# Optimization experiments

Hardware: AMD Instinct MI355X
Metric: run time of the kernel (lower is better)

Reference implementation:

```python
import jax, jax.numpy as jnp
import numpy as np

N_ATOMS = 20000
N_EDGES = 80000
ATOM_DIM = 29
BOND_DIM = 11
UNITS = 64
STEPS = 4
PAD = UNITS - ATOM_DIM  # 35


def setup_inputs() -> dict:
    key = jax.random.key(0)
    ks = jax.random.split(key, 8)
    atom_features = jax.random.normal(ks[0], (N_ATOMS, ATOM_DIM), dtype=jnp.float32)
    bond_features = jax.random.normal(ks[1], (N_EDGES, BOND_DIM), dtype=jnp.float32)
    pi = jax.random.randint(ks[2], (N_EDGES, 2), 0, N_ATOMS, dtype=jnp.int32)
    # tf.math.segment_sum in the original requires sorted segment ids
    order = jnp.argsort(pi[:, 0])
    pair_indices = pi[order]
    scale = 0.05
    edge_kernel = jax.random.normal(ks[3], (BOND_DIM, UNITS * UNITS), dtype=jnp.float32) * scale
    edge_bias = jnp.zeros((UNITS * UNITS,), dtype=jnp.float32)
    gru_kernel = jax.random.normal(ks[4], (UNITS, 3 * UNITS), dtype=jnp.float32) * scale
    gru_rec_kernel = jax.random.normal(ks[5], (UNITS, 3 * UNITS), dtype=jnp.float32) * scale
    gru_bias = jnp.zeros((2, 3 * UNITS), dtype=jnp.float32)
    return {
        "atom_features": atom_features,
        "bond_features": bond_features,
        "pair_indices": pair_indices,
        "edge_kernel": edge_kernel,
        "edge_bias": edge_bias,
        "gru_kernel": gru_kernel,
        "gru_rec_kernel": gru_rec_kernel,
        "gru_bias": gru_bias,
    }


def _edge_network(h, bond_features, pair_indices, edge_kernel, edge_bias):
    # per-edge learned transform: [E, bond_dim] -> [E, d, d]
    bf = bond_features @ edge_kernel + edge_bias
    bf = bf.reshape(-1, UNITS, UNITS)
    nbr = h[pair_indices[:, 1]]                      # gather neighbors [E, d]
    transformed = jnp.einsum('eij,ej->ei', bf, nbr)  # per-edge matvec
    # aggregate messages at target atoms (segment_sum)
    return jax.ops.segment_sum(transformed, pair_indices[:, 0], num_segments=N_ATOMS)


def _gru_cell(x, h, kernel, rec_kernel, bias):
    # keras GRUCell, reset_after=True
    xm = x @ kernel + bias[0]        # [N, 3u]
    hm = h @ rec_kernel + bias[1]    # [N, 3u]
    xz, xr, xh = jnp.split(xm, 3, axis=-1)
    rz, rr, rh = jnp.split(hm, 3, axis=-1)
    z = jax.nn.sigmoid(xz + rz)
    r = jax.nn.sigmoid(xr + rr)
    hh = jnp.tanh(xh + r * rh)
    return z * h + (1.0 - z) * hh


def reference(atom_features, bond_features, pair_indices, edge_kernel, edge_bias,
              gru_kernel, gru_rec_kernel, gru_bias):
    h = jnp.pad(atom_features, ((0, 0), (0, PAD)))
    for _ in range(STEPS):
        msg = _edge_network(h, bond_features, pair_indices, edge_kernel, edge_bias)
        h = _gru_cell(msg, h, gru_kernel, gru_rec_kernel, gru_bias)
    return h
```

## Files before the change

### kernel.cpp

```cpp
#include <hip/hip_runtime.h>

#define N_ATOMS 20000
#define N_EDGES 80000
#define ATOM_DIM 29
#define BOND_DIM 11
#define UNITS 64
#define STEPS 4
#define GCOLS 768
#define KTOT  832
#define BM    16
#define NTH   256
#define ASTRIDE 836
#define CT_MAIN 12
#define KT_MAIN 26
#define CT_RH 4
#define KT_RH 2
#define GSTRIDE 193
#define RSTRIDE 65

typedef _Float16 f16;
typedef __attribute__((ext_vector_type(8))) _Float16 f16x8;
typedef __attribute__((ext_vector_type(4))) float f32x4;

__global__ void init_h(const float* __restrict__ atom, float* __restrict__ h,
                       f16* __restrict__ h16) {
    int idx = blockIdx.x*256 + threadIdx.x;
    if (idx >= N_ATOMS*UNITS) return;
    int a = idx >> 6, i = idx & 63;
    float v = (i < ATOM_DIM) ? atom[a*ATOM_DIM + i] : 0.f;
    h[idx] = v;
    h16[idx] = (f16)v;
}

__global__ void build_rowptr(const int* __restrict__ pair, int* __restrict__ row_ptr) {
    int e = blockIdx.x*256 + threadIdx.x;
    if (e >= N_EDGES) return;
    int s = pair[2*e];
    if (e == 0) for (int a = 0; a <= s; a++) row_ptr[a] = 0;
    int snext = (e == N_EDGES-1) ? N_ATOMS : pair[2*(e+1)];
    for (int a = s+1; a <= snext; a++) row_ptr[a] = e+1;
}

__global__ void build_w3m(const float* __restrict__ ek, const float* __restrict__ eb,
                          const float* __restrict__ gk, const float* __restrict__ grk,
                          const float* __restrict__ gb, f16* __restrict__ W3m,
                          float* __restrict__ bias2) {
    int idx = blockIdx.x*256 + threadIdx.x;
    if (idx < 256) {
        int comp = idx >> 6, i = idx & 63;
        float b;
        if (comp == 0)      b = gb[i]       + gb[192 + i];
        else if (comp == 1) b = gb[64 + i]  + gb[256 + i];
        else if (comp == 2) b = gb[128 + i];
        else                b = gb[320 + i];
        bias2[idx] = b;
    }
    if (idx >= CT_MAIN*KT_MAIN*512) return;
    int t = idx >> 9, rem = idx & 511;
    int ct = t / KT_MAIN, kt = t % KT_MAIN;
    int lane = rem >> 3, e = rem & 7;
    int lq = lane >> 4, lr = lane & 15;
    int col = ct*16 + lr;
    int comp = col >> 6, i = col & 63;
    int k = kt*32 + lq*8 + e;
    float val = 0.f;
    if (k < GCOLS) {
        int b = k >> 6, q = k & 63;
        const float* E = (b < BOND_DIM) ? (ek + (size_t)b*4096 + q) : (eb + q);
        const float* T = gk + comp*64 + i;
        #pragma unroll 8
        for (int m = 0; m < 64; m++) val += E[m*64] * T[m*192];
    } else {
        int j = k - GCOLS;
        if (comp < 2) val = grk[j*192 + comp*64 + i];
    }
    W3m[idx] = (f16)val;
}

__global__ void build_w3r(const float* __restrict__ grk, f16* __restrict__ W3r) {
    int idx = blockIdx.x*256 + threadIdx.x;
    if (idx >= CT_RH*KT_RH*512) return;
    int t = idx >> 9, rem = idx & 511;
    int rt = t / KT_RH, kt = t % KT_RH;
    int lane = rem >> 3, e = rem & 7;
    int lq = lane >> 4, lr = lane & 15;
    int i = rt*16 + lr;
    int j = kt*32 + lq*8 + e;
    W3r[idx] = (f16)grk[j*192 + 128 + i];
}

__global__ __launch_bounds__(NTH, 5) void fused_step(
    const int* __restrict__ pair, const int* __restrict__ row_ptr,
    const float* __restrict__ bond, const f16* __restrict__ h16_in,
    f16* __restrict__ h16_out, const f16* __restrict__ W3m,
    const f16* __restrict__ W3r, const float* __restrict__ bias2,
    float* __restrict__ h) {
  __shared__ __align__(16) char smem[BM*ASTRIDE*2];
  f16 (*As)[ASTRIDE] = (f16 (*)[ASTRIDE])smem;
  float (*gates)[GSTRIDE] = (float (*)[GSTRIDE])smem;
  float (*rhb)[RSTRIDE] = (float (*)[RSTRIDE])(smem + BM*GSTRIDE*4);

  int a0 = blockIdx.x * BM;
  int tid = threadIdx.x;
  int lane = tid & 63, w = tid >> 6;
  int lq = lane >> 4, lr = lane & 15;

  const f16* bp[4];
  if (w < 3) {
    #pragma unroll
    for (int n=0;n<4;n++)
      bp[n] = W3m + ((size_t)(w*4 + n)*KT_MAIN)*512 + lane*8;
  } else {
    #pragma unroll
    for (int n=0;n<4;n++)
      bp[n] = W3r + ((size_t)n*KT_RH)*512 + lane*8;
  }
  f16x8 pb[4][2];
  #pragma unroll
  for (int n=0;n<4;n++) {
    pb[n][0] = *(const f16x8*)(bp[n]);
    pb[n][1] = *(const f16x8*)(bp[n] + 512);
  }

  for (int t = 0; t < 4; t++) {
    int r = w*4 + t;
    int a = a0 + r;
    int s = row_ptr[a], e_end = row_ptr[a+1];
    float g[BOND_DIM+1];
    #pragma unroll
    for (int b=0;b<=BOND_DIM;b++) g[b] = 0.f;
    int e = s;
    for (; e + 1 < e_end; e += 2) {
      int d0 = pair[2*e+1], d1 = pair[2*e+3];
      float h0 = (float)h16_in[(size_t)d0*UNITS + lane];
      float h1 = (float)h16_in[(size_t)d1*UNITS + lane];
      g[BOND_DIM] += h0 + h1;
      #pragma unroll
      for (int b=0;b<BOND_DIM;b++)
        g[b] += bond[(size_t)e*BOND_DIM + b]*h0 + bond[(size_t)(e+1)*BOND_DIM + b]*h1;
    }
    if (e < e_end) {
      int d0 = pair[2*e+1];
      float h0 = (float)h16_in[(size_t)d0*UNITS + lane];
      g[BOND_DIM] += h0;
      #pragma unroll
      for (int b=0;b<BOND_DIM;b++) g[b] += bond[(size_t)e*BOND_DIM + b]*h0;
    }
    #pragma unroll
    for (int b=0;b<=BOND_DIM;b++) As[r][b*64 + lane] = (f16)g[b];
    As[r][GCOLS + lane] = h16_in[(size_t)a*UNITS + lane];
  }

  int ei = tid & 63;
  float bz  = bias2[ei];
  float br  = bias2[64 + ei];
  float bxh = bias2[128 + ei];
  float brh = bias2[192 + ei];
  float hold[4];
  #pragma unroll
  for (int p=0;p<4;p++)
    hold[p] = h[(size_t)(a0 + (tid >> 6) + p*4)*UNITS + ei];

  __syncthreads();

  f32x4 acc[4];
  #pragma unroll
  for (int n=0;n<4;n++) acc[n] = (f32x4){0.f,0.f,0.f,0.f};

  if (w < 3) {
    #pragma unroll 2
    for (int kt = 0; kt < KT_MAIN; kt++) {
      f16x8 af = *(const f16x8*)&As[lr][kt*32 + lq*8];
      acc[0] = __builtin_amdgcn_mfma_f32_16x16x32_f16(af, pb[0][kt&1], acc[0], 0, 0, 0);
      acc[1] = __builtin_amdgcn_mfma_f32_16x16x32_f16(af, pb[1][kt&1], acc[1], 0, 0, 0);
      acc[2] = __builtin_amdgcn_mfma_f32_16x16x32_f16(af, pb[2][kt&1], acc[2], 0, 0, 0);
      acc[3] = __builtin_amdgcn_mfma_f32_16x16x32_f16(af, pb[3][kt&1], acc[3], 0, 0, 0);
      if (kt + 2 < KT_MAIN) {
        #pragma unroll
        for (int n=0;n<4;n++)
          pb[n][kt&1] = *(const f16x8*)(bp[n] + (size_t)(kt+2)*512);
      }
    }
  } else {
    #pragma unroll
    for (int kt = 0; kt < KT_RH; kt++) {
      f16x8 af = *(const f16x8*)&As[lr][GCOLS + kt*32 + lq*8];
      acc[0] = __builtin_amdgcn_mfma_f32_16x16x32_f16(af, pb[0][kt], acc[0], 0, 0, 0);
      acc[1] = __builtin_amdgcn_mfma_f32_16x16x32_f16(af, pb[1][kt], acc[1], 0, 0, 0);
      acc[2] = __builtin_amdgcn_mfma_f32_16x16x32_f16(af, pb[2][kt], acc[2], 0, 0, 0);
      acc[3] = __builtin_amdgcn_mfma_f32_16x16x32_f16(af, pb[3][kt], acc[3], 0, 0, 0);
    }
  }
  __syncthreads();

  if (w < 3) {
    #pragma unroll
    for (int n=0;n<4;n++) {
      int col = (w*4+n)*16 + lr;
      #pragma unroll
      for (int rr=0;rr<4;rr++)
        gates[lq*4 + rr][col] = acc[n][rr];
    }
  } else {
    #pragma unroll
    for (int n=0;n<4;n++) {
      int col = n*16 + lr;
      #pragma unroll
      for (int rr=0;rr<4;rr++)
        rhb[lq*4 + rr][col] = acc[n][rr];
    }
  }
  __syncthreads();

  #pragma unroll
  for (int p=0;p<4;p++) {
    int a_loc = (tid >> 6) + p*4;
    int a = a0 + a_loc;
    float zs = gates[a_loc][ei]        + bz;
    float rs = gates[a_loc][64 + ei]   + br;
    float xh = gates[a_loc][128 + ei]  + bxh;
    float rh = rhb[a_loc][ei]          + brh;
    float z  = 1.f/(1.f + __expf(-zs));
    float rg = 1.f/(1.f + __expf(-rs));
    float hh = tanhf(xh + rg*rh);
    float hn = z*hold[p] + (1.f - z)*hh;
    h[(size_t)a*UNITS + ei] = hn;
    h16_out[(size_t)a*UNITS + ei] = (f16)hn;
  }
}

extern "C" void kernel_launch(void* const* d_in, const int* in_sizes, int n_in,
                              void* d_out, int out_size, void* d_ws, size_t ws_size,
                              hipStream_t stream) {
  const float* atom  = (const float*)d_in[0];
  const float* bond  = (const float*)d_in[1];
  const int*   pair  = (const int*)d_in[2];
  const float* ek    = (const float*)d_in[3];
  const float* eb    = (const float*)d_in[4];
  const float* gk    = (const float*)d_in[5];
  const float* grk   = (const float*)d_in[6];
  const float* gbias = (const float*)d_in[7];

  float* h = (float*)d_out;

  char* w = (char*)d_ws;
  int*   row_ptr = (int*)w;        w += 80032;
  f16*   h16a    = (f16*)w;        w += (size_t)N_ATOMS*UNITS*2;
  f16*   h16b    = (f16*)w;        w += (size_t)N_ATOMS*UNITS*2;
  f16*   W3m     = (f16*)w;        w += (size_t)CT_MAIN*KT_MAIN*512*2;
  f16*   W3r     = (f16*)w;        w += (size_t)CT_RH*KT_RH*512*2;
  float* bias2   = (float*)w;      w += (size_t)256*4;

  init_h<<<(N_ATOMS*UNITS+255)/256, 256, 0, stream>>>(atom, h, h16a);
  build_rowptr<<<(N_EDGES+255)/256, 256, 0, stream>>>(pair, row_ptr);
  build_w3m<<<(CT_MAIN*KT_MAIN*512+255)/256, 256, 0, stream>>>(ek, eb, gk, grk, gbias, W3m, bias2);
  build_w3r<<<(CT_RH*KT_RH*512+255)/256, 256, 0, stream>>>(grk, W3r);

  f16* bufs[2] = { h16a, h16b };
  for (int s=0; s<STEPS; s++) {
    fused_step<<<N_ATOMS/BM, NTH, 0, stream>>>(
        pair, row_ptr, bond, bufs[s & 1], bufs[(s+1) & 1], W3m, W3r, bias2, h);
  }
}
```

Measured before the change: 194.7 us.

## Double atom tile per block to reuse weight fragments across two MFMA row tiles

```diff
diff --git a/kernel.cpp b/kernel.cpp
--- a/kernel.cpp
+++ b/kernel.cpp
@@ -8,7 +8,7 @@
 #define STEPS 4
 #define GCOLS 768
 #define KTOT  832
-#define BM    16
+#define BM    32
 #define NTH   256
 #define ASTRIDE 836
 #define CT_MAIN 12
@@ -89,7 +89,7 @@
     W3r[idx] = (f16)grk[j*192 + 128 + i];
 }
 
-__global__ __launch_bounds__(NTH, 5) void fused_step(
+__global__ __launch_bounds__(NTH, 3) void fused_step(
     const int* __restrict__ pair, const int* __restrict__ row_ptr,
     const float* __restrict__ bond, const f16* __restrict__ h16_in,
     f16* __restrict__ h16_out, const f16* __restrict__ W3m,
@@ -122,8 +122,8 @@
     pb[n][1] = *(const f16x8*)(bp[n] + 512);
   }
 
-  for (int t = 0; t < 4; t++) {
-    int r = w*4 + t;
+  for (int t = 0; t < 8; t++) {
+    int r = w*8 + t;
     int a = a0 + r;
     int s = row_ptr[a], e_end = row_ptr[a+1];
     float g[BOND_DIM+1];
@@ -156,25 +156,29 @@
   float br  = bias2[64 + ei];
   float bxh = bias2[128 + ei];
   float brh = bias2[192 + ei];
-  float hold[4];
-  #pragma unroll
-  for (int p=0;p<4;p++)
+  float hold[8];
+  #pragma unroll
+  for (int p=0;p<8;p++)
     hold[p] = h[(size_t)(a0 + (tid >> 6) + p*4)*UNITS + ei];
 
   __syncthreads();
 
-  f32x4 acc[4];
-  #pragma unroll
-  for (int n=0;n<4;n++) acc[n] = (f32x4){0.f,0.f,0.f,0.f};
+  f32x4 acc[2][4];
+  #pragma unroll
+  for (int m=0;m<2;m++)
+    #pragma unroll
+    for (int n=0;n<4;n++) acc[m][n] = (f32x4){0.f,0.f,0.f,0.f};
 
   if (w < 3) {
     #pragma unroll 2
     for (int kt = 0; kt < KT_MAIN; kt++) {
-      f16x8 af = *(const f16x8*)&As[lr][kt*32 + lq*8];
-      acc[0] = __builtin_amdgcn_mfma_f32_16x16x32_f16(af, pb[0][kt&1], acc[0], 0, 0, 0);
-      acc[1] = __builtin_amdgcn_mfma_f32_16x16x32_f16(af, pb[1][kt&1], acc[1], 0, 0, 0);
-      acc[2] = __builtin_amdgcn_mfma_f32_16x16x32_f16(af, pb[2][kt&1], acc[2], 0, 0, 0);
-      acc[3] = __builtin_amdgcn_mfma_f32_16x16x32_f16(af, pb[3][kt&1], acc[3], 0, 0, 0);
+      f16x8 af0 = *(const f16x8*)&As[lr][kt*32 + lq*8];
+      f16x8 af1 = *(const f16x8*)&As[16 + lr][kt*32 + lq*8];
+      #pragma unroll
+      for (int n=0;n<4;n++) {
+        acc[0][n] = __builtin_amdgcn_mfma_f32_16x16x32_f16(af0, pb[n][kt&1], acc[0][n], 0, 0, 0);
+        acc[1][n] = __builtin_amdgcn_mfma_f32_16x16x32_f16(af1, pb[n][kt&1], acc[1][n], 0, 0, 0);
+      }
       if (kt + 2 < KT_MAIN) {
         #pragma unroll
         for (int n=0;n<4;n++)
@@ -184,36 +188,42 @@
   } else {
     #pragma unroll
     for (int kt = 0; kt < KT_RH; kt++) {
-      f16x8 af = *(const f16x8*)&As[lr][GCOLS + kt*32 + lq*8];
-      acc[0] = __builtin_amdgcn_mfma_f32_16x16x32_f16(af, pb[0][kt], acc[0], 0, 0, 0);
-      acc[1] = __builtin_amdgcn_mfma_f32_16x16x32_f16(af, pb[1][kt], acc[1], 0, 0, 0);
-      acc[2] = __builtin_amdgcn_mfma_f32_16x16x32_f16(af, pb[2][kt], acc[2], 0, 0, 0);
-      acc[3] = __builtin_amdgcn_mfma_f32_16x16x32_f16(af, pb[3][kt], acc[3], 0, 0, 0);
+      f16x8 af0 = *(const f16x8*)&As[lr][GCOLS + kt*32 + lq*8];
+      f16x8 af1 = *(const f16x8*)&As[16 + lr][GCOLS + kt*32 + lq*8];
+      #pragma unroll
+      for (int n=0;n<4;n++) {
+        acc[0][n] = __builtin_amdgcn_mfma_f32_16x16x32_f16(af0, pb[n][kt], acc[0][n], 0, 0, 0);
+        acc[1][n] = __builtin_amdgcn_mfma_f32_16x16x32_f16(af1, pb[n][kt], acc[1][n], 0, 0, 0);
+      }
     }
   }
   __syncthreads();
 
   if (w < 3) {
     #pragma unroll
-    for (int n=0;n<4;n++) {
-      int col = (w*4+n)*16 + lr;
-      #pragma unroll
-      for (int rr=0;rr<4;rr++)
-        gates[lq*4 + rr][col] = acc[n][rr];
-    }
+    for (int m=0;m<2;m++)
+      #pragma unroll
+      for (int n=0;n<4;n++) {
+        int col = (w*4+n)*16 + lr;
+        #pragma unroll
+        for (int rr=0;rr<4;rr++)
+          gates[m*16 + lq*4 + rr][col] = acc[m][n][rr];
+      }
   } else {
     #pragma unroll
-    for (int n=0;n<4;n++) {
-      int col = n*16 + lr;
-      #pragma unroll
-      for (int rr=0;rr<4;rr++)
-        rhb[lq*4 + rr][col] = acc[n][rr];
-    }
+    for (int m=0;m<2;m++)
+      #pragma unroll
+      for (int n=0;n<4;n++) {
+        int col = n*16 + lr;
+        #pragma unroll
+        for (int rr=0;rr<4;rr++)
+          rhb[m*16 + lq*4 + rr][col] = acc[m][n][rr];
+      }
   }
   __syncthreads();
 
   #pragma unroll
-  for (int p=0;p<4;p++) {
+  for (int p=0;p<8;p++) {
     int a_loc = (tid >> 6) + p*4;
     int a = a0 + a_loc;
     float zs = gates[a_loc][ei]        + bz;
```

New measurement: 236.5 us. 1.21x slower.
